# Kernel optimization log

Hardware: AMD Instinct MI355X
Metric: run time of the kernel (lower is better)

Reference implementation:

```python
import jax, jax.numpy as jnp
import numpy as np

B, C, H, W_SP = 8, 2048, 28, 28   # last_conv feature map (ResNet-50, layer4 stride=1, 448px input)
D = 8192                          # count-sketch / CBP output dim
NUM_CLS = 200
L2_EPS = 1e-12                    # F.normalize default eps


def setup_inputs() -> dict:
    key = jax.random.key(0)
    ks = jax.random.split(key, 7)
    x = jax.random.normal(ks[0], (B, C, H, W_SP), dtype=jnp.float32)
    h1 = jax.random.randint(ks[1], (C,), 0, D, dtype=jnp.int32)
    h2 = jax.random.randint(ks[2], (C,), 0, D, dtype=jnp.int32)
    # Rademacher signs (count-sketch s vectors); map {0,1} -> {-1,+1}
    s1 = (2.0 * jax.random.bernoulli(ks[3], 0.5, (C,)).astype(jnp.float32) - 1.0)
    s2 = (2.0 * jax.random.bernoulli(ks[4], 0.5, (C,)).astype(jnp.float32) - 1.0)
    W_cls = jax.random.normal(ks[5], (D, NUM_CLS), dtype=jnp.float32) * 0.01
    b_cls = jnp.zeros((NUM_CLS,), dtype=jnp.float32)
    return {"x": x, "s1": s1, "s2": s2, "W_cls": W_cls, "b_cls": b_cls, "h1": h1, "h2": h2}


def _cbp_sum(xf, s1, s2, h1, h2):
    # xf: [B, L, C] per-pixel features.  Count-sketch each pixel twice, convolve
    # via FFT, then sum over all L spatial locations (== the original HxW loop).
    Bb, L, Cc = xf.shape
    sk1 = jnp.zeros((Bb, L, D), xf.dtype).at[..., h1].add(xf * s1)  # scatter-add over channels
    sk2 = jnp.zeros((Bb, L, D), xf.dtype).at[..., h2].add(xf * s2)
    f1 = jnp.fft.rfft(sk1, axis=-1)
    f2 = jnp.fft.rfft(sk2, axis=-1)
    y = jnp.fft.irfft(f1 * f2, n=D, axis=-1)  # [B, L, D] circular conv of sketches
    return y.sum(axis=1)                      # sum over spatial locations -> [B, D]


def reference(x, s1, s2, W_cls, b_cls, h1, h2):
    Bb, Cc, Hh, Ww = x.shape
    xf = x.transpose(0, 2, 3, 1).reshape(Bb, Hh * Ww, Cc)          # [B, L, C]
    y = _cbp_sum(xf, s1, s2, h1, h2)                               # [B, D]
    feat = jnp.sign(y) * jnp.sqrt(jnp.abs(y))                      # signed sqrt
    feat = feat / jnp.maximum(jnp.linalg.norm(feat, axis=1, keepdims=True), L2_EPS)
    logit = feat @ W_cls + b_cls
    return logit, feat
```

## Files before the change

### kernel.cpp

```cpp
#include <hip/hip_runtime.h>
#include <hip/hip_bf16.h>

#define BATCH 8
#define CH    2048
#define LSP   784
#define KPAD  832
#define KSTAGE 13
#define DDIM  8192
#define NCLS  200
#define NTILE 16
#define NPAIR 136
#define NSLOT 68
#define FXSCALE 8192.0f
#define FXINV   (1.0f/8192.0f)

typedef _Float16 f16x8 __attribute__((ext_vector_type(8)));
typedef _Float16 f16x4 __attribute__((ext_vector_type(4)));
typedef float    f32x4 __attribute__((ext_vector_type(4)));

#define FATOMIC(p, v) unsafeAtomicAdd((p), (v))

__global__ __launch_bounds__(256) void split_kernel(
    const float* __restrict__ x,
    _Float16* __restrict__ xh,
    float* __restrict__ part, float* __restrict__ norm,
    const float* __restrict__ s1, const int* __restrict__ h1,
    const float* __restrict__ s2, const int* __restrict__ h2,
    float4* __restrict__ metaG,
    const float* __restrict__ bc, float* __restrict__ out,
    int exclusive)
{
    int idx = blockIdx.x * 256 + threadIdx.x;
    if (!exclusive && idx < NSLOT * BATCH * DDIM / 4)
        *(float4*)&part[idx * 4] = make_float4(0.f, 0.f, 0.f, 0.f);
    if (idx < CH)
        metaG[idx] = make_float4(s1[idx] * 64.0f, __int_as_float(h1[idx]),
                                 s2[idx] * 128.0f, __int_as_float(h2[idx]));
    if (idx < BATCH) norm[idx] = 0.0f;
    if (idx < BATCH * NCLS) out[idx] = bc[idx % NCLS];
    if (idx >= BATCH * CH * KPAD / 8) return;
    int v  = idx * 8;
    int bc_ = v / KPAD;
    int l  = v - bc_ * KPAD;
    f16x8 hv = {0, 0, 0, 0, 0, 0, 0, 0};
    if (l < LSP) {
        const float* xp = &x[(size_t)bc_ * LSP + l];
        float4 a = *(const float4*)xp;
        float4 c = *(const float4*)(xp + 4);
        hv[0] = (_Float16)a.x; hv[1] = (_Float16)a.y;
        hv[2] = (_Float16)a.z; hv[3] = (_Float16)a.w;
        hv[4] = (_Float16)c.x; hv[5] = (_Float16)c.y;
        hv[6] = (_Float16)c.z; hv[7] = (_Float16)c.w;
    }
    *(f16x8*)&xh[v] = hv;
}

__device__ __forceinline__ void stage64(
    const _Float16* __restrict__ src,
    unsigned short* lds,
    int wv, int lane, int s)
{
    const int rowi = lane >> 3;
    const int gc   = (lane & 7) ^ rowi;
    const _Float16* g0 = src + (size_t)rowi * KPAD + s * 64 + gc * 8;
#pragma unroll
    for (int q = 0; q < 4; ++q) {
        const int r0 = wv * 32 + q * 8;
        __builtin_amdgcn_global_load_lds(
            (__attribute__((address_space(1))) void*)(g0 + (size_t)r0 * KPAD),
            (__attribute__((address_space(3))) void*)(lds + r0 * 64),
            16, 0, 0);
    }
}

__global__ __launch_bounds__(256, 2) void gram_scatter_kernel(
    const _Float16* __restrict__ xh,
    const float4* __restrict__ metaG,
    float* __restrict__ part,
    int exclusive)
{
    __shared__ __align__(16) unsigned short smA[128 * 64];
    __shared__ __align__(16) unsigned short smB[128 * 64];
    __shared__ __align__(16) int bins[DDIM];

    const int tid  = threadIdx.x;
    const int lane = tid & 63;
    const int wv   = tid >> 6;
    const int b    = blockIdx.x & 7;
    const int pgrp = blockIdx.x >> 3;

    for (int i = tid; i < DDIM; i += 256) bins[i] = 0;

    const int wrow = (wv >> 1) * 64;
    const int wcol = (wv & 1) * 64;
    const int rsel = lane & 15;
    const int khi  = lane >> 4;

#pragma unroll 1
    for (int pp = 0; pp < 2; ++pp) {
        const int pidx = pgrp + pp * NSLOT;

        int tM = 0, tN = 0;
        {
            int i = pidx;
#pragma unroll 1
            for (int t = 0; t < NTILE; ++t) {
                int cnt = NTILE - t;
                if (i < cnt) { tM = t; tN = t + i; break; }
                i -= cnt;
            }
        }
        const bool diag = (tM == tN);

        const _Float16* srcA = xh + ((size_t)b * CH + (size_t)tM * 128) * KPAD;
        const _Float16* srcB = xh + ((size_t)b * CH + (size_t)tN * 128) * KPAD;
        const unsigned short* fragB = diag ? smA : smB;

        f32x4 acc[4][4];
        const f32x4 zv = {0.0f, 0.0f, 0.0f, 0.0f};
#pragma unroll
        for (int mi = 0; mi < 4; ++mi)
#pragma unroll
            for (int ni = 0; ni < 4; ++ni) acc[mi][ni] = zv;

#pragma unroll 1
        for (int s = 0; s < KSTAGE; ++s) {
            stage64(srcA, smA, wv, lane, s);
            if (!diag) stage64(srcB, smB, wv, lane, s);
            __syncthreads();
#pragma unroll
            for (int t = 0; t < 2; ++t) {
                const int co = ((((t << 2) + khi) ^ (rsel & 7)) << 3);
                f16x8 ah[4], bh[4];
#pragma unroll
                for (int i = 0; i < 4; ++i) {
                    ah[i] = *(const f16x8*)&smA[(wrow + i * 16 + rsel) * 64 + co];
                    bh[i] = *(const f16x8*)&fragB[(wcol + i * 16 + rsel) * 64 + co];
                }
#pragma unroll
                for (int mi = 0; mi < 4; ++mi)
#pragma unroll
                    for (int ni = 0; ni < 4; ++ni)
                        acc[mi][ni] = __builtin_amdgcn_mfma_f32_16x16x32_f16(
                            ah[mi], bh[ni], acc[mi][ni], 0, 0, 0);
            }
            __syncthreads();
        }

        const int c2b = tN * 128 + wcol + rsel;
        int   h1c[4], h2c[4]; float s1c[4], s2c[4];
#pragma unroll
        for (int ni = 0; ni < 4; ++ni) {
            float4 cm = metaG[c2b + ni * 16];
            s1c[ni] = cm.x; h1c[ni] = __float_as_int(cm.y);
            s2c[ni] = cm.z; h2c[ni] = __float_as_int(cm.w);
        }

        const int rowbase = tM * 128 + wrow + (khi << 2);
#pragma unroll
        for (int mi = 0; mi < 4; ++mi) {
            float4 rm[4];
#pragma unroll
            for (int r = 0; r < 4; ++r) rm[r] = metaG[rowbase + mi * 16 + r];
#pragma unroll
            for (int r = 0; r < 4; ++r) {
                const float s1r = rm[r].x, s2r = rm[r].z;
                const int h1r = __float_as_int(rm[r].y);
                const int h2r = __float_as_int(rm[r].w);
#pragma unroll
                for (int ni = 0; ni < 4; ++ni) {
                    float g = acc[mi][ni][r];
                    atomicAdd(&bins[(h1r + h2c[ni]) & (DDIM - 1)],
                              (int)(s1r * s2c[ni] * g));
                    if (!diag)
                        atomicAdd(&bins[(h1c[ni] + h2r) & (DDIM - 1)],
                                  (int)(s1c[ni] * s2r * g));
                }
            }
        }
    }

    __syncthreads();

    if (exclusive) {
        float* pbase = part + ((size_t)(pgrp * BATCH + b) * DDIM);
#pragma unroll 4
        for (int i = tid; i < DDIM / 4; i += 256) {
            int4 v = *(const int4*)&bins[i * 4];
            float4 f = make_float4((float)v.x * FXINV, (float)v.y * FXINV,
                                   (float)v.z * FXINV, (float)v.w * FXINV);
            *(float4*)&pbase[i * 4] = f;
        }
    } else {
        float* pbase = part + ((size_t)(pgrp * BATCH + b) * DDIM);
        const int rot = (blockIdx.x & 31) << 8;
        for (int i = tid; i < DDIM; i += 256) {
            int j = (i + rot) & (DDIM - 1);
            int v = bins[j];
            if (v != 0) FATOMIC(&pbase[j], (float)v * FXINV);
        }
    }
}

__global__ __launch_bounds__(256) void reduce_kernel(
    const float* __restrict__ part, float* __restrict__ y,
    float* __restrict__ norm)
{
    const int tid = threadIdx.x;
    const int b   = blockIdx.x & 7;
    const int d0  = (blockIdx.x >> 3) * 256 + tid;
    float s = 0.0f;
#pragma unroll 4
    for (int p = 0; p < NSLOT; ++p)
        s += part[((size_t)p * BATCH + b) * DDIM + d0];
    y[(size_t)b * DDIM + d0] = s;
    float ab = fabsf(s);
    __shared__ float red[256];
    red[tid] = ab;
    __syncthreads();
    for (int st = 128; st > 0; st >>= 1) {
        if (tid < st) red[tid] += red[tid + st];
        __syncthreads();
    }
    if (tid == 0) FATOMIC(&norm[b], red[0]);
}

__global__ __launch_bounds__(256) void logit_kernel(
    const float* __restrict__ y, const float* __restrict__ norm,
    const float* __restrict__ W, float* __restrict__ out)
{
    const int j = blockIdx.x;
    const int tid = threadIdx.x;
    __shared__ float fs[BATCH][128];
    for (int i = tid; i < BATCH * 128; i += 256) {
        int bb = i >> 7, dd = i & 127;
        float v = y[(size_t)bb * DDIM + j * 128 + dd];
        float inv = 1.0f / fmaxf(sqrtf(norm[bb]), 1e-12f);
        float f = copysignf(sqrtf(fabsf(v)), v) * inv;
        fs[bb][dd] = f;
        out[BATCH * NCLS + (size_t)bb * DDIM + j * 128 + dd] = f;
    }
    __syncthreads();
    if (tid < NCLS) {
        float a[BATCH];
#pragma unroll
        for (int bb = 0; bb < BATCH; ++bb) a[bb] = 0.0f;
        for (int dd = 0; dd < 128; ++dd) {
            float w = W[(size_t)(j * 128 + dd) * NCLS + tid];
#pragma unroll
            for (int bb = 0; bb < BATCH; ++bb) a[bb] += fs[bb][dd] * w;
        }
#pragma unroll
        for (int bb = 0; bb < BATCH; ++bb)
            FATOMIC(&out[bb * NCLS + tid], a[bb]);
    }
}

extern "C" void kernel_launch(void* const* d_in, const int* in_sizes, int n_in,
                              void* d_out, int out_size, void* d_ws, size_t ws_size,
                              hipStream_t stream)
{
    const float* x  = (const float*)d_in[0];
    const float* s1 = (const float*)d_in[1];
    const float* s2 = (const float*)d_in[2];
    const float* W  = (const float*)d_in[3];
    const float* bc = (const float*)d_in[4];
    const int*   h1 = (const int*)d_in[5];
    const int*   h2 = (const int*)d_in[6];
    float* out = (float*)d_out;

    const size_t ybytes  = (size_t)BATCH * DDIM * sizeof(float);
    const size_t xhbytes = (size_t)BATCH * CH * KPAD * sizeof(_Float16);

    const size_t partbytes = (size_t)NSLOT * BATCH * DDIM * sizeof(float);
    const int exclusive = (ws_size >= partbytes + ybytes + 128 + xhbytes);

    char* ws = (char*)d_ws;
    float* part = (float*)ws;
    float* y    = (float*)(ws + partbytes);
    float4* metaG = (float4*)(ws + partbytes);
    float* norm = (float*)(ws + partbytes + ybytes);
    _Float16* xh = (_Float16*)(ws + partbytes + ybytes + 128);

    split_kernel<<<(BATCH * CH * KPAD / 8 + 255) / 256, 256, 0, stream>>>(
        x, xh, part, norm, s1, h1, s2, h2, metaG, bc, out, exclusive);

    gram_scatter_kernel<<<NSLOT * BATCH, 256, 0, stream>>>(
        xh, metaG, part, exclusive);

    reduce_kernel<<<256, 256, 0, stream>>>(part, y, norm);

    logit_kernel<<<64, 256, 0, stream>>>(y, norm, W, out);
}
```

Baseline: 185.8 us.

## Double-buffer K tiles and give each block a single tile pair

```diff
diff --git a/kernel.cpp b/kernel.cpp
--- a/kernel.cpp
+++ b/kernel.cpp
@@ -5,7 +5,7 @@
 #define CH    2048
 #define LSP   784
 #define KPAD  832
-#define KSTAGE 13
+#define KSTEPS 26
 #define DDIM  8192
 #define NCLS  200
 #define NTILE 16
@@ -55,20 +55,20 @@
     *(f16x8*)&xh[v] = hv;
 }
 
-__device__ __forceinline__ void stage64(
+__device__ __forceinline__ void stage_tile(
     const _Float16* __restrict__ src,
-    unsigned short* lds,
-    int wv, int lane, int s)
-{
-    const int rowi = lane >> 3;
-    const int gc   = (lane & 7) ^ rowi;
-    const _Float16* g0 = src + (size_t)rowi * KPAD + s * 64 + gc * 8;
-#pragma unroll
-    for (int q = 0; q < 4; ++q) {
-        const int r0 = wv * 32 + q * 8;
+    unsigned short* lds_tile,
+    int wv, int lane, int k0)
+{
+#pragma unroll
+    for (int half = 0; half < 2; ++half) {
+        int ch  = wv * 2 + half;
+        int row = ch * 16 + (lane >> 2);
+        int kg  = (lane & 3) ^ ((lane >> 3) & 3);
+        const _Float16* g = src + (size_t)row * KPAD + k0 + kg * 8;
         __builtin_amdgcn_global_load_lds(
-            (__attribute__((address_space(1))) void*)(g0 + (size_t)r0 * KPAD),
-            (__attribute__((address_space(3))) void*)(lds + r0 * 64),
+            (__attribute__((address_space(1))) void*)g,
+            (__attribute__((address_space(3))) void*)(lds_tile + ch * 512),
             16, 0, 0);
     }
 }
@@ -79,111 +79,121 @@
     float* __restrict__ part,
     int exclusive)
 {
-    __shared__ __align__(16) unsigned short smA[128 * 64];
-    __shared__ __align__(16) unsigned short smB[128 * 64];
+    __shared__ __align__(16) unsigned short smA[2][128 * 32];
+    __shared__ __align__(16) unsigned short smB[2][128 * 32];
     __shared__ __align__(16) int bins[DDIM];
 
     const int tid  = threadIdx.x;
     const int lane = tid & 63;
     const int wv   = tid >> 6;
     const int b    = blockIdx.x & 7;
-    const int pgrp = blockIdx.x >> 3;
+    const int pidx = blockIdx.x >> 3;
 
     for (int i = tid; i < DDIM; i += 256) bins[i] = 0;
+
+    int tM = 0, tN = 0;
+    {
+        int i = pidx;
+#pragma unroll 1
+        for (int t = 0; t < NTILE; ++t) {
+            int cnt = NTILE - t;
+            if (i < cnt) { tM = t; tN = t + i; break; }
+            i -= cnt;
+        }
+    }
+    const bool diag = (tM == tN);
 
     const int wrow = (wv >> 1) * 64;
     const int wcol = (wv & 1) * 64;
     const int rsel = lane & 15;
     const int khi  = lane >> 4;
 
+    const _Float16* srcA = xh + ((size_t)b * CH + (size_t)tM * 128) * KPAD;
+    const _Float16* srcB = xh + ((size_t)b * CH + (size_t)tN * 128) * KPAD;
+
+    f32x4 acc[4][4];
+    const f32x4 zv = {0.0f, 0.0f, 0.0f, 0.0f};
+#pragma unroll
+    for (int mi = 0; mi < 4; ++mi)
+#pragma unroll
+        for (int ni = 0; ni < 4; ++ni) acc[mi][ni] = zv;
+
+    const int fxor = ((khi ^ ((lane >> 1) & 3)) << 3);
+
+    stage_tile(srcA, smA[0], wv, lane, 0);
+    if (!diag) stage_tile(srcB, smB[0], wv, lane, 0);
+
 #pragma unroll 1
-    for (int pp = 0; pp < 2; ++pp) {
-        const int pidx = pgrp + pp * NSLOT;
-
-        int tM = 0, tN = 0;
-        {
-            int i = pidx;
-#pragma unroll 1
-            for (int t = 0; t < NTILE; ++t) {
-                int cnt = NTILE - t;
-                if (i < cnt) { tM = t; tN = t + i; break; }
-                i -= cnt;
+    for (int s = 0; s < KSTEPS; ++s) {
+        const int cur = s & 1;
+        if (s + 1 < KSTEPS) {
+            stage_tile(srcA, smA[cur ^ 1], wv, lane, (s + 1) * 32);
+            if (!diag) stage_tile(srcB, smB[cur ^ 1], wv, lane, (s + 1) * 32);
+            __builtin_amdgcn_sched_barrier(0);
+            if (diag) asm volatile("s_waitcnt vmcnt(2)" ::: "memory");
+            else      asm volatile("s_waitcnt vmcnt(4)" ::: "memory");
+        } else {
+            __builtin_amdgcn_sched_barrier(0);
+            asm volatile("s_waitcnt vmcnt(0)" ::: "memory");
+        }
+        __builtin_amdgcn_s_barrier();
+        __builtin_amdgcn_sched_barrier(0);
+
+        const unsigned short* bufA = smA[cur];
+        const unsigned short* bufB = diag ? smA[cur] : smB[cur];
+        f16x8 ah[4], bh[4];
+#pragma unroll
+        for (int i = 0; i < 4; ++i) {
+            ah[i] = *(const f16x8*)&bufA[(wrow + i * 16 + rsel) * 32 + fxor];
+            bh[i] = *(const f16x8*)&bufB[(wcol + i * 16 + rsel) * 32 + fxor];
+        }
+#pragma unroll
+        for (int mi = 0; mi < 4; ++mi)
+#pragma unroll
+            for (int ni = 0; ni < 4; ++ni)
+                acc[mi][ni] = __builtin_amdgcn_mfma_f32_16x16x32_f16(
+                    ah[mi], bh[ni], acc[mi][ni], 0, 0, 0);
+
+        __builtin_amdgcn_sched_barrier(0);
+        __builtin_amdgcn_s_barrier();
+    }
+
+    const int c2b = tN * 128 + wcol + rsel;
+    int   h1c[4], h2c[4]; float s1c[4], s2c[4];
+#pragma unroll
+    for (int ni = 0; ni < 4; ++ni) {
+        float4 cm = metaG[c2b + ni * 16];
+        s1c[ni] = cm.x; h1c[ni] = __float_as_int(cm.y);
+        s2c[ni] = cm.z; h2c[ni] = __float_as_int(cm.w);
+    }
+
+    const int rowbase = tM * 128 + wrow + (khi << 2);
+#pragma unroll
+    for (int mi = 0; mi < 4; ++mi) {
+        float4 rm[4];
+#pragma unroll
+        for (int r = 0; r < 4; ++r) rm[r] = metaG[rowbase + mi * 16 + r];
+#pragma unroll
+        for (int r = 0; r < 4; ++r) {
+            const float s1r = rm[r].x, s2r = rm[r].z;
+            const int h1r = __float_as_int(rm[r].y);
+            const int h2r = __float_as_int(rm[r].w);
+#pragma unroll
+            for (int ni = 0; ni < 4; ++ni) {
+                float g = acc[mi][ni][r];
+                atomicAdd(&bins[(h1r + h2c[ni]) & (DDIM - 1)],
+                          (int)(s1r * s2c[ni] * g));
+                if (!diag)
+                    atomicAdd(&bins[(h1c[ni] + h2r) & (DDIM - 1)],
+                              (int)(s1c[ni] * s2r * g));
             }
         }
-        const bool diag = (tM == tN);
-
-        const _Float16* srcA = xh + ((size_t)b * CH + (size_t)tM * 128) * KPAD;
-        const _Float16* srcB = xh + ((size_t)b * CH + (size_t)tN * 128) * KPAD;
-        const unsigned short* fragB = diag ? smA : smB;
-
-        f32x4 acc[4][4];
-        const f32x4 zv = {0.0f, 0.0f, 0.0f, 0.0f};
-#pragma unroll
-        for (int mi = 0; mi < 4; ++mi)
-#pragma unroll
-            for (int ni = 0; ni < 4; ++ni) acc[mi][ni] = zv;
-
-#pragma unroll 1
-        for (int s = 0; s < KSTAGE; ++s) {
-            stage64(srcA, smA, wv, lane, s);
-            if (!diag) stage64(srcB, smB, wv, lane, s);
-            __syncthreads();
-#pragma unroll
-            for (int t = 0; t < 2; ++t) {
-                const int co = ((((t << 2) + khi) ^ (rsel & 7)) << 3);
-                f16x8 ah[4], bh[4];
-#pragma unroll
-                for (int i = 0; i < 4; ++i) {
-                    ah[i] = *(const f16x8*)&smA[(wrow + i * 16 + rsel) * 64 + co];
-                    bh[i] = *(const f16x8*)&fragB[(wcol + i * 16 + rsel) * 64 + co];
-                }
-#pragma unroll
-                for (int mi = 0; mi < 4; ++mi)
-#pragma unroll
-                    for (int ni = 0; ni < 4; ++ni)
-                        acc[mi][ni] = __builtin_amdgcn_mfma_f32_16x16x32_f16(
-                            ah[mi], bh[ni], acc[mi][ni], 0, 0, 0);
-            }
-            __syncthreads();
-        }
-
-        const int c2b = tN * 128 + wcol + rsel;
-        int   h1c[4], h2c[4]; float s1c[4], s2c[4];
-#pragma unroll
-        for (int ni = 0; ni < 4; ++ni) {
-            float4 cm = metaG[c2b + ni * 16];
-            s1c[ni] = cm.x; h1c[ni] = __float_as_int(cm.y);
-            s2c[ni] = cm.z; h2c[ni] = __float_as_int(cm.w);
-        }
-
-        const int rowbase = tM * 128 + wrow + (khi << 2);
-#pragma unroll
-        for (int mi = 0; mi < 4; ++mi) {
-            float4 rm[4];
-#pragma unroll
-            for (int r = 0; r < 4; ++r) rm[r] = metaG[rowbase + mi * 16 + r];
-#pragma unroll
-            for (int r = 0; r < 4; ++r) {
-                const float s1r = rm[r].x, s2r = rm[r].z;
-                const int h1r = __float_as_int(rm[r].y);
-                const int h2r = __float_as_int(rm[r].w);
-#pragma unroll
-                for (int ni = 0; ni < 4; ++ni) {
-                    float g = acc[mi][ni][r];
-                    atomicAdd(&bins[(h1r + h2c[ni]) & (DDIM - 1)],
-                              (int)(s1r * s2c[ni] * g));
-                    if (!diag)
-                        atomicAdd(&bins[(h1c[ni] + h2r) & (DDIM - 1)],
-                                  (int)(s1c[ni] * s2r * g));
-                }
-            }
-        }
     }
 
     __syncthreads();
 
     if (exclusive) {
-        float* pbase = part + ((size_t)(pgrp * BATCH + b) * DDIM);
+        float* pbase = part + ((size_t)(pidx * BATCH + b) * DDIM);
 #pragma unroll 4
         for (int i = tid; i < DDIM / 4; i += 256) {
             int4 v = *(const int4*)&bins[i * 4];
@@ -192,7 +202,7 @@
             *(float4*)&pbase[i * 4] = f;
         }
     } else {
-        float* pbase = part + ((size_t)(pgrp * BATCH + b) * DDIM);
+        float* pbase = part + ((size_t)((pidx % NSLOT) * BATCH + b) * DDIM);
         const int rot = (blockIdx.x & 31) << 8;
         for (int i = tid; i < DDIM; i += 256) {
             int j = (i + rot) & (DDIM - 1);
@@ -204,14 +214,14 @@
 
 __global__ __launch_bounds__(256) void reduce_kernel(
     const float* __restrict__ part, float* __restrict__ y,
-    float* __restrict__ norm)
+    float* __restrict__ norm, int nslots)
 {
     const int tid = threadIdx.x;
     const int b   = blockIdx.x & 7;
     const int d0  = (blockIdx.x >> 3) * 256 + tid;
     float s = 0.0f;
-#pragma unroll 4
-    for (int p = 0; p < NSLOT; ++p)
+#pragma unroll 8
+    for (int p = 0; p < nslots; ++p)
         s += part[((size_t)p * BATCH + b) * DDIM + d0];
     y[(size_t)b * DDIM + d0] = s;
     float ab = fabsf(s);
@@ -272,8 +282,11 @@
     const size_t ybytes  = (size_t)BATCH * DDIM * sizeof(float);
     const size_t xhbytes = (size_t)BATCH * CH * KPAD * sizeof(_Float16);
 
-    const size_t partbytes = (size_t)NSLOT * BATCH * DDIM * sizeof(float);
-    const int exclusive = (ws_size >= partbytes + ybytes + 128 + xhbytes);
+    size_t partbytes = (size_t)NPAIR * BATCH * DDIM * sizeof(float);
+    int exclusive = (ws_size >= partbytes + ybytes + 128 + xhbytes);
+    if (!exclusive)
+        partbytes = (size_t)NSLOT * BATCH * DDIM * sizeof(float);
+    const int nslots = exclusive ? NPAIR : NSLOT;
 
     char* ws = (char*)d_ws;
     float* part = (float*)ws;
@@ -285,10 +298,10 @@
     split_kernel<<<(BATCH * CH * KPAD / 8 + 255) / 256, 256, 0, stream>>>(
         x, xh, part, norm, s1, h1, s2, h2, metaG, bc, out, exclusive);
 
-    gram_scatter_kernel<<<NSLOT * BATCH, 256, 0, stream>>>(
+    gram_scatter_kernel<<<NPAIR * BATCH, 256, 0, stream>>>(
         xh, metaG, part, exclusive);
 
-    reduce_kernel<<<256, 256, 0, stream>>>(part, y, norm);
+    reduce_kernel<<<256, 256, 0, stream>>>(part, y, norm, nslots);
 
     logit_kernel<<<64, 256, 0, stream>>>(y, norm, W, out);
 }
```

Measured after the change: 192.8 us. 1.04x slower.

## Launch one gram block per tile pair instead of two pairs per block

Applied to the files above, without the earlier changes.

```diff
diff --git a/kernel.cpp b/kernel.cpp
--- a/kernel.cpp
+++ b/kernel.cpp
@@ -87,103 +87,98 @@
     const int lane = tid & 63;
     const int wv   = tid >> 6;
     const int b    = blockIdx.x & 7;
-    const int pgrp = blockIdx.x >> 3;
+    const int pidx = blockIdx.x >> 3;
 
     for (int i = tid; i < DDIM; i += 256) bins[i] = 0;
+
+    int tM = 0, tN = 0;
+    {
+        int i = pidx;
+#pragma unroll 1
+        for (int t = 0; t < NTILE; ++t) {
+            int cnt = NTILE - t;
+            if (i < cnt) { tM = t; tN = t + i; break; }
+            i -= cnt;
+        }
+    }
+    const bool diag = (tM == tN);
 
     const int wrow = (wv >> 1) * 64;
     const int wcol = (wv & 1) * 64;
     const int rsel = lane & 15;
     const int khi  = lane >> 4;
 
+    const _Float16* srcA = xh + ((size_t)b * CH + (size_t)tM * 128) * KPAD;
+    const _Float16* srcB = xh + ((size_t)b * CH + (size_t)tN * 128) * KPAD;
+    const unsigned short* fragB = diag ? smA : smB;
+
+    f32x4 acc[4][4];
+    const f32x4 zv = {0.0f, 0.0f, 0.0f, 0.0f};
+#pragma unroll
+    for (int mi = 0; mi < 4; ++mi)
+#pragma unroll
+        for (int ni = 0; ni < 4; ++ni) acc[mi][ni] = zv;
+
 #pragma unroll 1
-    for (int pp = 0; pp < 2; ++pp) {
-        const int pidx = pgrp + pp * NSLOT;
-
-        int tM = 0, tN = 0;
-        {
-            int i = pidx;
-#pragma unroll 1
-            for (int t = 0; t < NTILE; ++t) {
-                int cnt = NTILE - t;
-                if (i < cnt) { tM = t; tN = t + i; break; }
-                i -= cnt;
+    for (int s = 0; s < KSTAGE; ++s) {
+        stage64(srcA, smA, wv, lane, s);
+        if (!diag) stage64(srcB, smB, wv, lane, s);
+        __syncthreads();
+#pragma unroll
+        for (int t = 0; t < 2; ++t) {
+            const int co = ((((t << 2) + khi) ^ (rsel & 7)) << 3);
+            f16x8 ah[4], bh[4];
+#pragma unroll
+            for (int i = 0; i < 4; ++i) {
+                ah[i] = *(const f16x8*)&smA[(wrow + i * 16 + rsel) * 64 + co];
+                bh[i] = *(const f16x8*)&fragB[(wcol + i * 16 + rsel) * 64 + co];
             }
-        }
-        const bool diag = (tM == tN);
-
-        const _Float16* srcA = xh + ((size_t)b * CH + (size_t)tM * 128) * KPAD;
-        const _Float16* srcB = xh + ((size_t)b * CH + (size_t)tN * 128) * KPAD;
-        const unsigned short* fragB = diag ? smA : smB;
-
-        f32x4 acc[4][4];
-        const f32x4 zv = {0.0f, 0.0f, 0.0f, 0.0f};
-#pragma unroll
-        for (int mi = 0; mi < 4; ++mi)
-#pragma unroll
-            for (int ni = 0; ni < 4; ++ni) acc[mi][ni] = zv;
-
-#pragma unroll 1
-        for (int s = 0; s < KSTAGE; ++s) {
-            stage64(srcA, smA, wv, lane, s);
-            if (!diag) stage64(srcB, smB, wv, lane, s);
-            __syncthreads();
-#pragma unroll
-            for (int t = 0; t < 2; ++t) {
-                const int co = ((((t << 2) + khi) ^ (rsel & 7)) << 3);
-                f16x8 ah[4], bh[4];
-#pragma unroll
-                for (int i = 0; i < 4; ++i) {
-                    ah[i] = *(const f16x8*)&smA[(wrow + i * 16 + rsel) * 64 + co];
-                    bh[i] = *(const f16x8*)&fragB[(wcol + i * 16 + rsel) * 64 + co];
-                }
-#pragma unroll
-                for (int mi = 0; mi < 4; ++mi)
-#pragma unroll
-                    for (int ni = 0; ni < 4; ++ni)
-                        acc[mi][ni] = __builtin_amdgcn_mfma_f32_16x16x32_f16(
-                            ah[mi], bh[ni], acc[mi][ni], 0, 0, 0);
+#pragma unroll
+            for (int mi = 0; mi < 4; ++mi)
+#pragma unroll
+                for (int ni = 0; ni < 4; ++ni)
+                    acc[mi][ni] = __builtin_amdgcn_mfma_f32_16x16x32_f16(
+                        ah[mi], bh[ni], acc[mi][ni], 0, 0, 0);
+        }
+        __syncthreads();
+    }
+
+    const int c2b = tN * 128 + wcol + rsel;
+    int   h1c[4], h2c[4]; float s1c[4], s2c[4];
+#pragma unroll
+    for (int ni = 0; ni < 4; ++ni) {
+        float4 cm = metaG[c2b + ni * 16];
+        s1c[ni] = cm.x; h1c[ni] = __float_as_int(cm.y);
+        s2c[ni] = cm.z; h2c[ni] = __float_as_int(cm.w);
+    }
+
+    const int rowbase = tM * 128 + wrow + (khi << 2);
+#pragma unroll
+    for (int mi = 0; mi < 4; ++mi) {
+        float4 rm[4];
+#pragma unroll
+        for (int r = 0; r < 4; ++r) rm[r] = metaG[rowbase + mi * 16 + r];
+#pragma unroll
+        for (int r = 0; r < 4; ++r) {
+            const float s1r = rm[r].x, s2r = rm[r].z;
+            const int h1r = __float_as_int(rm[r].y);
+            const int h2r = __float_as_int(rm[r].w);
+#pragma unroll
+            for (int ni = 0; ni < 4; ++ni) {
+                float g = acc[mi][ni][r];
+                atomicAdd(&bins[(h1r + h2c[ni]) & (DDIM - 1)],
+                          (int)(s1r * s2c[ni] * g));
+                if (!diag)
+                    atomicAdd(&bins[(h1c[ni] + h2r) & (DDIM - 1)],
+                              (int)(s1c[ni] * s2r * g));
             }
-            __syncthreads();
-        }
-
-        const int c2b = tN * 128 + wcol + rsel;
-        int   h1c[4], h2c[4]; float s1c[4], s2c[4];
-#pragma unroll
-        for (int ni = 0; ni < 4; ++ni) {
-            float4 cm = metaG[c2b + ni * 16];
-            s1c[ni] = cm.x; h1c[ni] = __float_as_int(cm.y);
-            s2c[ni] = cm.z; h2c[ni] = __float_as_int(cm.w);
-        }
-
-        const int rowbase = tM * 128 + wrow + (khi << 2);
-#pragma unroll
-        for (int mi = 0; mi < 4; ++mi) {
-            float4 rm[4];
-#pragma unroll
-            for (int r = 0; r < 4; ++r) rm[r] = metaG[rowbase + mi * 16 + r];
-#pragma unroll
-            for (int r = 0; r < 4; ++r) {
-                const float s1r = rm[r].x, s2r = rm[r].z;
-                const int h1r = __float_as_int(rm[r].y);
-                const int h2r = __float_as_int(rm[r].w);
-#pragma unroll
-                for (int ni = 0; ni < 4; ++ni) {
-                    float g = acc[mi][ni][r];
-                    atomicAdd(&bins[(h1r + h2c[ni]) & (DDIM - 1)],
-                              (int)(s1r * s2c[ni] * g));
-                    if (!diag)
-                        atomicAdd(&bins[(h1c[ni] + h2r) & (DDIM - 1)],
-                                  (int)(s1c[ni] * s2r * g));
-                }
-            }
         }
     }
 
     __syncthreads();
 
     if (exclusive) {
-        float* pbase = part + ((size_t)(pgrp * BATCH + b) * DDIM);
+        float* pbase = part + ((size_t)(pidx * BATCH + b) * DDIM);
 #pragma unroll 4
         for (int i = tid; i < DDIM / 4; i += 256) {
             int4 v = *(const int4*)&bins[i * 4];
@@ -192,7 +187,7 @@
             *(float4*)&pbase[i * 4] = f;
         }
     } else {
-        float* pbase = part + ((size_t)(pgrp * BATCH + b) * DDIM);
+        float* pbase = part + ((size_t)((pidx % NSLOT) * BATCH + b) * DDIM);
         const int rot = (blockIdx.x & 31) << 8;
         for (int i = tid; i < DDIM; i += 256) {
             int j = (i + rot) & (DDIM - 1);
@@ -204,14 +199,14 @@
 
 __global__ __launch_bounds__(256) void reduce_kernel(
     const float* __restrict__ part, float* __restrict__ y,
-    float* __restrict__ norm)
+    float* __restrict__ norm, int nslots)
 {
     const int tid = threadIdx.x;
     const int b   = blockIdx.x & 7;
     const int d0  = (blockIdx.x >> 3) * 256 + tid;
     float s = 0.0f;
-#pragma unroll 4
-    for (int p = 0; p < NSLOT; ++p)
+#pragma unroll 8
+    for (int p = 0; p < nslots; ++p)
         s += part[((size_t)p * BATCH + b) * DDIM + d0];
     y[(size_t)b * DDIM + d0] = s;
     float ab = fabsf(s);
@@ -231,22 +226,24 @@
 {
     const int j = blockIdx.x;
     const int tid = threadIdx.x;
-    __shared__ float fs[BATCH][128];
-    for (int i = tid; i < BATCH * 128; i += 256) {
-        int bb = i >> 7, dd = i & 127;
-        float v = y[(size_t)bb * DDIM + j * 128 + dd];
-        float inv = 1.0f / fmaxf(sqrtf(norm[bb]), 1e-12f);
-        float f = copysignf(sqrtf(fabsf(v)), v) * inv;
+    __shared__ float fs[BATCH][64];
+    __shared__ float inv[BATCH];
+    if (tid < BATCH) inv[tid] = 1.0f / fmaxf(sqrtf(norm[tid]), 1e-12f);
+    __syncthreads();
+    for (int i = tid; i < BATCH * 64; i += 256) {
+        int bb = i >> 6, dd = i & 63;
+        float v = y[(size_t)bb * DDIM + j * 64 + dd];
+        float f = copysignf(sqrtf(fabsf(v)), v) * inv[bb];
         fs[bb][dd] = f;
-        out[BATCH * NCLS + (size_t)bb * DDIM + j * 128 + dd] = f;
+        out[BATCH * NCLS + (size_t)bb * DDIM + j * 64 + dd] = f;
     }
     __syncthreads();
     if (tid < NCLS) {
         float a[BATCH];
 #pragma unroll
         for (int bb = 0; bb < BATCH; ++bb) a[bb] = 0.0f;
-        for (int dd = 0; dd < 128; ++dd) {
-            float w = W[(size_t)(j * 128 + dd) * NCLS + tid];
+        for (int dd = 0; dd < 64; ++dd) {
+            float w = W[(size_t)(j * 64 + dd) * NCLS + tid];
 #pragma unroll
             for (int bb = 0; bb < BATCH; ++bb) a[bb] += fs[bb][dd] * w;
         }
@@ -272,8 +269,11 @@
     const size_t ybytes  = (size_t)BATCH * DDIM * sizeof(float);
     const size_t xhbytes = (size_t)BATCH * CH * KPAD * sizeof(_Float16);
 
-    const size_t partbytes = (size_t)NSLOT * BATCH * DDIM * sizeof(float);
-    const int exclusive = (ws_size >= partbytes + ybytes + 128 + xhbytes);
+    size_t partbytes = (size_t)NPAIR * BATCH * DDIM * sizeof(float);
+    int exclusive = (ws_size >= partbytes + ybytes + 128 + xhbytes);
+    if (!exclusive)
+        partbytes = (size_t)NSLOT * BATCH * DDIM * sizeof(float);
+    const int nslots = exclusive ? NPAIR : NSLOT;
 
     char* ws = (char*)d_ws;
     float* part = (float*)ws;
@@ -285,10 +285,10 @@
     split_kernel<<<(BATCH * CH * KPAD / 8 + 255) / 256, 256, 0, stream>>>(
         x, xh, part, norm, s1, h1, s2, h2, metaG, bc, out, exclusive);
 
-    gram_scatter_kernel<<<NSLOT * BATCH, 256, 0, stream>>>(
+    gram_scatter_kernel<<<NPAIR * BATCH, 256, 0, stream>>>(
         xh, metaG, part, exclusive);
 
-    reduce_kernel<<<256, 256, 0, stream>>>(part, y, norm);
-
-    logit_kernel<<<64, 256, 0, stream>>>(y, norm, W, out);
-}
+    reduce_kernel<<<256, 256, 0, stream>>>(part, y, norm, nslots);
+
+    logit_kernel<<<128, 256, 0, stream>>>(y, norm, W, out);
+}
```

Measured after the change: 176.0 us. 5.3% less time.
